# Kernel optimization log

Hardware: AMD Instinct MI355X
Metric: run time of the kernel (lower is better)

Reference implementation:

```python
import jax, jax.numpy as jnp
import numpy as np

# --- batched state-vector quantum circuit sim: AngleEmbedding(RY) + BasicEntanglerLayers(RX + ring CNOT) ---

def _ry(state, theta, wire, n):
    # per-sample RY(theta) on `wire`; state: (B,) + (2,)*n complex
    ax = wire + 1
    c = jnp.cos(0.5 * theta).reshape((-1,) + (1,) * (n - 1)).astype(state.dtype)
    s = jnp.sin(0.5 * theta).reshape((-1,) + (1,) * (n - 1)).astype(state.dtype)
    s0 = jnp.take(state, 0, axis=ax)
    s1 = jnp.take(state, 1, axis=ax)
    return jnp.stack([c * s0 - s * s1, s * s0 + c * s1], axis=ax)

def _rx(state, theta, wire, n):
    # scalar RX(theta) on `wire` (shared weight across batch)
    ax = wire + 1
    c = jnp.cos(0.5 * theta).astype(state.dtype)
    s = (-1j * jnp.sin(0.5 * theta)).astype(state.dtype)
    s0 = jnp.take(state, 0, axis=ax)
    s1 = jnp.take(state, 1, axis=ax)
    return jnp.stack([c * s0 + s * s1, s * s0 + c * s1], axis=ax)

def _cnot(state, ctrl, tgt):
    ax_c = ctrl + 1
    s0 = jnp.take(state, 0, axis=ax_c)
    s1 = jnp.take(state, 1, axis=ax_c)
    ax_t = tgt + 1 if tgt < ctrl else tgt  # target axis index after removing ctrl axis
    s1 = jnp.flip(s1, axis=ax_t)
    return jnp.stack([s0, s1], axis=ax_c)

def _circuit(x_qin, qweights):
    # x_qin: (Bn, n) angles; qweights: (L, n)
    Bn, n = x_qin.shape
    state = jnp.zeros((Bn,) + (2,) * n, jnp.complex64)
    state = state.at[(slice(None),) + (0,) * n].set(1.0)
    for w in range(n):  # AngleEmbedding, rotation='Y'
        state = _ry(state, x_qin[:, w], w, n)
    for l in range(qweights.shape[0]):  # BasicEntanglerLayers
        for w in range(n):
            state = _rx(state, qweights[l, w], w, n)
        for w in range(n):
            state = _cnot(state, w, (w + 1) % n)
    probs = jnp.real(state * jnp.conj(state))
    outs = []
    for w in range(n):  # <Z_w> = P(bit_w=0) - P(bit_w=1)
        axes = tuple(a for a in range(1, n + 1) if a != w + 1)
        p = probs.sum(axis=axes)  # (Bn, 2)
        outs.append(p[:, 0] - p[:, 1])
    return jnp.stack(outs, axis=-1).astype(jnp.float32)


def setup_inputs() -> dict:
    key = jax.random.key(0)
    ks = jax.random.split(key, 9)
    B, N, H, NQ, L = 16, 1024, 256, 8, 2
    x = jax.random.normal(ks[0], (B, N, H), jnp.float32)
    norm_adj = jax.random.uniform(ks[1], (N, N), jnp.float32) / N
    Wg = jax.random.normal(ks[2], (H, H), jnp.float32) * 0.02
    bg = jax.random.normal(ks[3], (H,), jnp.float32) * 0.02
    Wpre = jax.random.normal(ks[4], (NQ, H), jnp.float32) * 0.05
    bpre = jax.random.normal(ks[5], (NQ,), jnp.float32) * 0.02
    qweights = jax.random.uniform(ks[6], (L, NQ), jnp.float32) * (2.0 * np.pi)
    Wpost = jax.random.normal(ks[7], (H, NQ), jnp.float32) * 0.1
    bpost = jax.random.normal(ks[8], (H,), jnp.float32) * 0.02
    return {"x": x, "norm_adj": norm_adj, "Wg": Wg, "bg": bg, "Wpre": Wpre,
            "bpre": bpre, "qweights": qweights, "Wpost": Wpost, "bpost": bpost}


def reference(x, norm_adj, Wg, bg, Wpre, bpre, qweights, Wpost, bpost):
    # GCN aggregation + GELU(Linear)  (dropout is identity in eval mode)
    x_agg = jnp.einsum('ij,bjh->bih', norm_adj, x)
    x_agg = jax.nn.gelu(x_agg @ Wg.T + bg, approximate=False)
    B, N, H = x_agg.shape
    x_flat = x_agg.reshape(B * N, H).astype(jnp.float32)
    x_qin = jnp.tanh(x_flat @ Wpre.T + bpre) * np.pi
    q_out = _circuit(x_qin, qweights)          # (B*N, n_qubits)
    out = (q_out @ Wpost.T + bpost).reshape(B, N, H)
    return out
```

## Files before the change

kernel.cpp:

```cpp
#include <hip/hip_runtime.h>
#include <math.h>

typedef __attribute__((ext_vector_type(8))) short bf16x8;
typedef _Float16 f16x8 __attribute__((ext_vector_type(8)));
typedef __attribute__((ext_vector_type(4))) float f32x4;

#define PI_F 3.14159265358979323846f

__device__ __forceinline__ unsigned short f2bf(float f) {
  unsigned int u = __float_as_uint(f);
  u += 0x7FFFu + ((u >> 16) & 1u);
  return (unsigned short)(u >> 16);
}

__device__ __forceinline__ float bf2f(unsigned short u) {
  return __uint_as_float(((unsigned int)u) << 16);
}

__device__ __forceinline__ void async_ld16(const unsigned short* g, unsigned short* l) {
  __builtin_amdgcn_global_load_lds(
      (const __attribute__((address_space(1))) void*)g,
      (__attribute__((address_space(3))) void*)l,
      16, 0, 0);
}

__device__ __forceinline__ float fast_erf(float x) {
  float a = fabsf(x);
  float t = 1.0f / fmaf(0.3275911f, a, 1.0f);
  float p = t * fmaf(t, fmaf(t, fmaf(t, fmaf(t, 1.061405429f, -1.453152027f),
                                     1.421413741f), -0.284496736f), 0.254829592f);
  float e = __expf(-a * a);
  float r = 1.0f - p * e;
  return copysignf(r, x);
}

__device__ __forceinline__ float fast_tanh(float a) {
  float e = __expf(2.0f * a);
  return 1.0f - 2.0f / (e + 1.0f);
}

template<int ML, int MR>
__device__ __forceinline__ void apply_rx(float re[4], float im[4], float c, float s) {
  float pr[4], pi[4];
  #pragma unroll
  for (int r = 0; r < 4; r++) {
    float vr = re[r ^ MR], vi = im[r ^ MR];
    if (ML) { vr = __shfl_xor(vr, ML, 64); vi = __shfl_xor(vi, ML, 64); }
    pr[r] = vr; pi[r] = vi;
  }
  #pragma unroll
  for (int r = 0; r < 4; r++) {
    re[r] = fmaf(c, re[r],  s * pi[r]);
    im[r] = fmaf(c, im[r], -s * pr[r]);
  }
}

__device__ __forceinline__ void fold_reduce8(float v[8], int L) {
  #pragma unroll
  for (int step = 0; step < 3; step++) {
    int d = 1 << step;
    int half = 4 >> step;
    bool hi = (L & d) != 0;
    #pragma unroll
    for (int w = 0; w < half; w++) {
      float send = hi ? v[w] : v[w + half];
      float recv = __shfl_xor(send, d, 64);
      v[w] = (hi ? v[w + half] : v[w]) + recv;
    }
  }
  v[0] += __shfl_xor(v[0], 8, 64);
  v[0] += __shfl_xor(v[0], 16, 64);
  v[0] += __shfl_xor(v[0], 32, 64);
}

__global__ __launch_bounds__(256)
void prep_kernel(const float* __restrict__ adj, unsigned short* __restrict__ adj_bf,
                 const float* __restrict__ Wg, unsigned short* __restrict__ Wg_bf,
                 const float* __restrict__ qw, unsigned short* __restrict__ Uri,
                 const float* __restrict__ Wpost, _Float16* __restrict__ Gt,
                 const float* __restrict__ x, unsigned short* __restrict__ xT) {
  __shared__ float smem[1056];
  int bid = blockIdx.x, t = threadIdx.x;
  if (bid < 1024) {
    int i = bid * 256 + t;
    float4 v = ((const float4*)adj)[i];
    ushort4 o; o.x = f2bf(v.x); o.y = f2bf(v.y); o.z = f2bf(v.z); o.w = f2bf(v.w);
    ((ushort4*)adj_bf)[i] = o;
  } else if (bid < 1088) {
    int i = (bid - 1024) * 256 + t;
    float4 v = ((const float4*)Wg)[i];
    ushort4 o; o.x = f2bf(v.x); o.y = f2bf(v.y); o.z = f2bf(v.z); o.w = f2bf(v.w);
    ((ushort4*)Wg_bf)[i] = o;
  } else if (bid < 1152) {
    if (t < 16) { smem[t] = cosf(0.5f * qw[t]); smem[16 + t] = sinf(0.5f * qw[t]); }
    __syncthreads();
    int wv = t >> 6, L = t & 63;
    int k = (bid - 1088) * 4 + wv;
    float re[4], im[4];
    #pragma unroll
    for (int r = 0; r < 4; r++) { re[r] = (r * 64 + L == k) ? 1.f : 0.f; im[r] = 0.f; }
    apply_rx<1, 0>(re, im, smem[0], smem[16]);
    apply_rx<2, 0>(re, im, smem[1], smem[17]);
    apply_rx<4, 0>(re, im, smem[2], smem[18]);
    apply_rx<8, 0>(re, im, smem[3], smem[19]);
    apply_rx<16, 0>(re, im, smem[4], smem[20]);
    apply_rx<32, 0>(re, im, smem[5], smem[21]);
    apply_rx<0, 1>(re, im, smem[6], smem[22]);
    apply_rx<0, 2>(re, im, smem[7], smem[23]);
    apply_rx<3, 0>(re, im, smem[8], smem[24]);
    apply_rx<6, 0>(re, im, smem[9], smem[25]);
    apply_rx<12, 0>(re, im, smem[10], smem[26]);
    apply_rx<24, 0>(re, im, smem[11], smem[27]);
    apply_rx<48, 0>(re, im, smem[12], smem[28]);
    apply_rx<32, 1>(re, im, smem[13], smem[29]);
    apply_rx<0, 3>(re, im, smem[14], smem[30]);
    apply_rx<3, 2>(re, im, smem[15], smem[31]);
    const int M[8] = {0xAB, 0xFD, 0xFA, 0xF5, 0xEA, 0xD5, 0xAA, 0x55};
    #pragma unroll
    for (int r = 0; r < 4; r++) {
      int n = 0;
      #pragma unroll
      for (int w = 0; w < 8; w++) {
        int bit = (__popc(L & (M[w] & 63)) ^ __popc((r << 6) & M[w])) & 1;
        n |= bit << w;
      }
      int row_re = ((n >> 4) << 5) + (n & 15);
      Uri[(size_t)row_re * 256 + k] = f2bf(re[r]);
      Uri[(size_t)(row_re + 16) * 256 + k] = f2bf(im[r]);
    }
  } else if (bid < 1168) {
    int tid = (bid - 1152) * 256 + t;
    int h = tid >> 4;
    int n0 = (tid & 15) << 4;
    float wv8[8];
    #pragma unroll
    for (int w = 0; w < 8; w++) wv8[w] = Wpost[h * 8 + w];
    #pragma unroll
    for (int j = 0; j < 16; j++) {
      int n = n0 + j;
      float sum = 0.f;
      #pragma unroll
      for (int w = 0; w < 8; w++) sum += ((n >> w) & 1) ? -wv8[w] : wv8[w];
      Gt[h * 256 + n] = (_Float16)sum;
    }
  } else {
    int tb = bid - 1168;
    int jt = tb & 31, ht = (tb >> 5) & 7, bb = tb >> 8;
    int tx = t & 31, ty = t >> 5;
    const float* xb = x + (size_t)bb * 1024 * 256;
    #pragma unroll
    for (int i = 0; i < 4; i++) {
      int j = jt * 32 + ty + i * 8;
      smem[(ty + i * 8) * 33 + tx] = xb[(size_t)j * 256 + ht * 32 + tx];
    }
    __syncthreads();
    unsigned short* xTb = xT + (size_t)bb * 256 * 1024;
    #pragma unroll
    for (int i = 0; i < 4; i++) {
      int h = ht * 32 + ty + i * 8;
      xTb[(size_t)h * 1024 + jt * 32 + tx] = f2bf(smem[tx * 33 + ty + i * 8]);
    }
  }
}

__global__ __launch_bounds__(256)
void gemm1_kernel(const unsigned short* __restrict__ A,
                  const unsigned short* __restrict__ Bt,
                  unsigned short* __restrict__ C,
                  int K, int tilesN, int ldC) {
  __shared__ unsigned short As[2 * 128 * 32];
  __shared__ unsigned short Bs[2 * 64 * 32];
  int rr  = blockIdx.x;
  int im  = rr / tilesN;
  int in_ = rr % tilesN;
  const unsigned short* Ab  = A  + (long long)im * 128 * K;
  const unsigned short* Btb = Bt + (long long)in_ * 64 * K;

  int t = threadIdx.x;
  int wv = t >> 6, lane = t & 63;
  int wm = wv >> 1, wn = wv & 1;
  int l15 = lane & 15, quad = lane >> 4;

  f32x4 acc[4][2] = {};

  for (int kk = 0; kk < K; kk += 64) {
    __syncthreads();
    #pragma unroll
    for (int kb = 0; kb < 2; kb++) {
      #pragma unroll
      for (int q = 0; q < 2; q++) {
        int ch = q * 256 + t;
        async_ld16(Ab + (long long)(ch >> 2) * K + kk + kb * 32 + (ch & 3) * 8,
                   &As[kb * 4096 + ch * 8]);
      }
      {
        int ch = t;
        async_ld16(Btb + (long long)(ch >> 2) * K + kk + kb * 32 + (ch & 3) * 8,
                   &Bs[kb * 2048 + ch * 8]);
      }
    }
    __syncthreads();
    #pragma unroll
    for (int kb = 0; kb < 2; kb++) {
      bf16x8 af[4], bfr[2];
      #pragma unroll
      for (int mt = 0; mt < 4; mt++)
        af[mt] = *(const bf16x8*)&As[kb * 4096 + (wm * 64 + mt * 16 + l15) * 32 + quad * 8];
      #pragma unroll
      for (int nt = 0; nt < 2; nt++)
        bfr[nt] = *(const bf16x8*)&Bs[kb * 2048 + (wn * 32 + nt * 16 + l15) * 32 + quad * 8];
      #pragma unroll
      for (int mt = 0; mt < 4; mt++)
        #pragma unroll
        for (int nt = 0; nt < 2; nt++)
          acc[mt][nt] = __builtin_amdgcn_mfma_f32_16x16x32_bf16(af[mt], bfr[nt], acc[mt][nt], 0, 0, 0);
    }
  }

  int n0 = in_ * 64;
  #pragma unroll
  for (int mt = 0; mt < 4; mt++) {
    #pragma unroll
    for (int nt = 0; nt < 2; nt++) {
      int colg = n0 + wn * 32 + nt * 16 + l15;
      #pragma unroll
      for (int r = 0; r < 4; r++) {
        int rowg = im * 128 + wm * 64 + mt * 16 + quad * 4 + r;
        C[(size_t)rowg * ldC + colg] = f2bf(acc[mt][nt][r]);
      }
    }
  }
}

__global__ __launch_bounds__(256)
void qfused_kernel(const unsigned short* __restrict__ xagg,
                   const unsigned short* __restrict__ Wg,
                   const float* __restrict__ bg,
                   const float* __restrict__ Wpre, const float* __restrict__ bpre,
                   const unsigned short* __restrict__ Uri,
                   const _Float16* __restrict__ Gt,
                   const float* __restrict__ bpost,
                   float* __restrict__ out) {
  __shared__ __align__(16) char smemraw[75776];
  unsigned short* As    = (unsigned short*)smemraw;
  unsigned short* Bs    = (unsigned short*)(smemraw + 2048);
  unsigned short* gs    = (unsigned short*)(smemraw + 34816);
  _Float16*       Ts    = (_Float16*)(smemraw + 34816);
  unsigned short* P0s   = (unsigned short*)(smemraw + 51200);
  float*          sWpre = (float*)(smemraw + 67584);

  int t = threadIdx.x;
  int wv = t >> 6, lane = t & 63;
  int l15 = lane & 15, quad = lane >> 4;

  for (int i = t; i < 2048; i += 256) sWpre[i] = Wpre[i];

  const unsigned short* Ab = xagg + (size_t)blockIdx.x * 32 * 256;

  f32x4 acc[2][4] = {};
  for (int kk = 0; kk < 256; kk += 32) {
    __syncthreads();
    if (wv < 2)
      async_ld16(Ab + (size_t)(wv * 16 + (lane >> 2)) * 256 + kk + (lane & 3) * 8,
                 &As[(wv * 16) * 32]);
    #pragma unroll
    for (int rd = 0; rd < 4; rd++) {
      int n = wv * 64 + rd * 16 + (lane >> 2);
      async_ld16(Wg + (size_t)n * 256 + kk + (lane & 3) * 8,
                 &Bs[(wv * 64 + rd * 16) * 32]);
    }
    __syncthreads();
    bf16x8 af[2], bfr[4];
    #pragma unroll
    for (int mt = 0; mt < 2; mt++)
      af[mt] = *(const bf16x8*)&As[(mt * 16 + l15) * 32 + quad * 8];
    #pragma unroll
    for (int nt = 0; nt < 4; nt++)
      bfr[nt] = *(const bf16x8*)&Bs[(wv * 64 + nt * 16 + l15) * 32 + quad * 8];
    #pragma unroll
    for (int mt = 0; mt < 2; mt++)
      #pragma unroll
      for (int nt = 0; nt < 4; nt++)
        acc[mt][nt] = __builtin_amdgcn_mfma_f32_16x16x32_bf16(af[mt], bfr[nt], acc[mt][nt], 0, 0, 0);
  }
  #pragma unroll
  for (int mt = 0; mt < 2; mt++) {
    #pragma unroll
    for (int nt = 0; nt < 4; nt++) {
      int col = wv * 64 + nt * 16 + l15;
      float bgl = bg[col];
      #pragma unroll
      for (int r = 0; r < 4; r++) {
        int row = mt * 16 + quad * 4 + r;
        float v = acc[mt][nt][r] + bgl;
        v = 0.5f * v * (1.0f + fast_erf(v * 0.7071067811865475f));
        gs[row * 256 + col] = f2bf(v);
      }
    }
  }
  __syncthreads();

  #pragma unroll
  for (int rr = 0; rr < 8; rr++) {
    int row = wv * 8 + rr;
    ushort4 gu = *(const ushort4*)&gs[row * 256 + 4 * lane];
    float g0 = bf2f(gu.x), g1 = bf2f(gu.y), g2 = bf2f(gu.z), g3 = bf2f(gu.w);
    float ang[8];
    #pragma unroll
    for (int w = 0; w < 8; w++) {
      float4 wp = *(const float4*)&sWpre[w * 256 + 4 * lane];
      float a = g0 * wp.x;
      a = fmaf(g1, wp.y, a);
      a = fmaf(g2, wp.z, a);
      a = fmaf(g3, wp.w, a);
      ang[w] = a;
    }
    fold_reduce8(ang, lane);
    float angf[8];
    #pragma unroll
    for (int w = 0; w < 8; w++) {
      int src = ((w >> 2) & 1) | (w & 2) | ((w & 1) << 2);
      angf[w] = __shfl(ang[0], src, 64);
    }
    float cw[8], sw[8];
    #pragma unroll
    for (int w = 0; w < 8; w++) {
      float th = (0.5f * PI_F) * fast_tanh(angf[w] + bpre[w]);
      cw[w] = __cosf(th); sw[w] = __sinf(th);
    }
    float pl = 1.f;
    #pragma unroll
    for (int bbit = 0; bbit < 6; bbit++) pl *= ((lane >> bbit) & 1) ? sw[bbit + 2] : cw[bbit + 2];
    ushort4 o;
    o.x = f2bf(pl * cw[0] * cw[1]);
    o.y = f2bf(pl * sw[0] * cw[1]);
    o.z = f2bf(pl * cw[0] * sw[1]);
    o.w = f2bf(pl * sw[0] * sw[1]);
    *(ushort4*)&P0s[(lane >> 3) * 1024 + row * 32 + 4 * (lane & 7)] = o;
  }

  f32x4 acc1[2][8] = {};
  for (int kk = 0; kk < 256; kk += 32) {
    __syncthreads();
    #pragma unroll
    for (int rd = 0; rd < 8; rd++) {
      int n = wv * 128 + rd * 16 + (lane >> 2);
      async_ld16(Uri + (size_t)n * 256 + kk + (lane & 3) * 8,
                 &Bs[(wv * 128 + rd * 16) * 32]);
    }
    __syncthreads();
    bf16x8 af[2], bfr[8];
    #pragma unroll
    for (int mt = 0; mt < 2; mt++)
      af[mt] = *(const bf16x8*)&P0s[(kk >> 5) * 1024 + (mt * 16 + l15) * 32 + quad * 8];
    #pragma unroll
    for (int nt = 0; nt < 8; nt++)
      bfr[nt] = *(const bf16x8*)&Bs[(wv * 128 + nt * 16 + l15) * 32 + quad * 8];
    #pragma unroll
    for (int mt = 0; mt < 2; mt++)
      #pragma unroll
      for (int nt = 0; nt < 8; nt++)
        acc1[mt][nt] = __builtin_amdgcn_mfma_f32_16x16x32_bf16(af[mt], bfr[nt], acc1[mt][nt], 0, 0, 0);
  }

  #pragma unroll
  for (int mt = 0; mt < 2; mt++) {
    #pragma unroll
    for (int p = 0; p < 4; p++) {
      int kb = wv * 2 + (p >> 1);
      int cip = (p & 1) * 16 + l15;
      #pragma unroll
      for (int r = 0; r < 4; r++) {
        int row = mt * 16 + quad * 4 + r;
        float tre = acc1[mt][2 * p][r], tim = acc1[mt][2 * p + 1][r];
        Ts[kb * 1024 + row * 32 + cip] = (_Float16)(tre * tre + tim * tim);
      }
    }
  }

  f32x4 acc2[2][4] = {};
  for (int kk = 0; kk < 256; kk += 32) {
    __syncthreads();
    #pragma unroll
    for (int rd = 0; rd < 4; rd++) {
      int h = wv * 64 + rd * 16 + (lane >> 2);
      async_ld16((const unsigned short*)Gt + (size_t)h * 256 + kk + (lane & 3) * 8,
                 &Bs[(wv * 64 + rd * 16) * 32]);
    }
    __syncthreads();
    f16x8 af[2], bfr[4];
    #pragma unroll
    for (int mt = 0; mt < 2; mt++)
      af[mt] = *(const f16x8*)&Ts[(kk >> 5) * 1024 + (mt * 16 + l15) * 32 + quad * 8];
    #pragma unroll
    for (int nt = 0; nt < 4; nt++)
      bfr[nt] = *(const f16x8*)&Bs[(wv * 64 + nt * 16 + l15) * 32 + quad * 8];
    #pragma unroll
    for (int mt = 0; mt < 2; mt++)
      #pragma unroll
      for (int nt = 0; nt < 4; nt++)
        acc2[mt][nt] = __builtin_amdgcn_mfma_f32_16x16x32_f16(af[mt], bfr[nt], acc2[mt][nt], 0, 0, 0);
  }

  #pragma unroll
  for (int mt = 0; mt < 2; mt++) {
    #pragma unroll
    for (int nt = 0; nt < 4; nt++) {
      int col = wv * 64 + nt * 16 + l15;
      float bp = bpost[col];
      #pragma unroll
      for (int r = 0; r < 4; r++) {
        int row = mt * 16 + quad * 4 + r;
        int s = blockIdx.x * 32 + row;
        int orow = (s & 15) * 1024 + (s >> 4);
        out[(size_t)orow * 256 + col] = acc2[mt][nt][r] + bp;
      }
    }
  }
}

extern "C" void kernel_launch(void* const* d_in, const int* in_sizes, int n_in,
                              void* d_out, int out_size, void* d_ws, size_t ws_size,
                              hipStream_t stream) {
  const float* x     = (const float*)d_in[0];
  const float* adj   = (const float*)d_in[1];
  const float* Wg    = (const float*)d_in[2];
  const float* bg    = (const float*)d_in[3];
  const float* Wpre  = (const float*)d_in[4];
  const float* bpre  = (const float*)d_in[5];
  const float* qw    = (const float*)d_in[6];
  const float* Wpost = (const float*)d_in[7];
  const float* bpost = (const float*)d_in[8];
  float* out = (float*)d_out;

  char* ws = (char*)d_ws;
  unsigned short* adj_bf  = (unsigned short*)(ws + 0);
  unsigned short* Wg_bf   = (unsigned short*)(ws + 2097152);
  unsigned short* xT_bf   = (unsigned short*)(ws + 2228224);
  unsigned short* xagg_bf = (unsigned short*)(ws + 10616832);
  unsigned short* Uri     = (unsigned short*)(ws + 19005440);
  _Float16*       Gt      = (_Float16*)(ws + 19267584);

  prep_kernel<<<5264, 256, 0, stream>>>(adj, adj_bf, Wg, Wg_bf, qw, Uri,
                                        Wpost, Gt, x, xT_bf);

  gemm1_kernel<<<512, 256, 0, stream>>>(adj_bf, xT_bf, xagg_bf, 1024, 64, 4096);

  qfused_kernel<<<512, 256, 0, stream>>>(xagg_bf, Wg_bf, bg, Wpre, bpre, Uri, Gt, bpost, out);
}
```

Measured before the change: 146.9 us.

## Load GEMM operands directly from global into registers with double buffering, swizzle LDS

In the fused quantum kernel, the three GEMM stages now load their B-operand weights (and the A operand of the first stage) straight from global memory into registers, double-buffered one k-step ahead. This replaces the async global-to-LDS copies and the two barriers per k-step. Wpre is held in registers rather than LDS, and tanh/cos/sin is computed once per lane and then shuffled instead of being repeated eight times per lane. The P0 and T intermediate LDS tiles use an XOR swizzle to reduce bank conflicts, and LDS use drops from about 74KB to 32KB, which may allow more blocks per CU at the cost of higher register pressure and uncoalesced weight loads that depend on L2 hits.

```diff
diff --git a/kernel.cpp b/kernel.cpp
--- a/kernel.cpp
+++ b/kernel.cpp
@@ -241,47 +241,43 @@
                    const _Float16* __restrict__ Gt,
                    const float* __restrict__ bpost,
                    float* __restrict__ out) {
-  __shared__ __align__(16) char smemraw[75776];
-  unsigned short* As    = (unsigned short*)smemraw;
-  unsigned short* Bs    = (unsigned short*)(smemraw + 2048);
-  unsigned short* gs    = (unsigned short*)(smemraw + 34816);
-  _Float16*       Ts    = (_Float16*)(smemraw + 34816);
-  unsigned short* P0s   = (unsigned short*)(smemraw + 51200);
-  float*          sWpre = (float*)(smemraw + 67584);
+  __shared__ __align__(16) char smemraw[32768];
+  unsigned short* gs  = (unsigned short*)smemraw;
+  _Float16*       Ts  = (_Float16*)smemraw;
+  unsigned short* P0s = (unsigned short*)(smemraw + 16384);
 
   int t = threadIdx.x;
   int wv = t >> 6, lane = t & 63;
   int l15 = lane & 15, quad = lane >> 4;
 
-  for (int i = t; i < 2048; i += 256) sWpre[i] = Wpre[i];
-
   const unsigned short* Ab = xagg + (size_t)blockIdx.x * 32 * 256;
 
   f32x4 acc[2][4] = {};
-  for (int kk = 0; kk < 256; kk += 32) {
-    __syncthreads();
-    if (wv < 2)
-      async_ld16(Ab + (size_t)(wv * 16 + (lane >> 2)) * 256 + kk + (lane & 3) * 8,
-                 &As[(wv * 16) * 32]);
-    #pragma unroll
-    for (int rd = 0; rd < 4; rd++) {
-      int n = wv * 64 + rd * 16 + (lane >> 2);
-      async_ld16(Wg + (size_t)n * 256 + kk + (lane & 3) * 8,
-                 &Bs[(wv * 64 + rd * 16) * 32]);
-    }
-    __syncthreads();
-    bf16x8 af[2], bfr[4];
-    #pragma unroll
-    for (int mt = 0; mt < 2; mt++)
-      af[mt] = *(const bf16x8*)&As[(mt * 16 + l15) * 32 + quad * 8];
-    #pragma unroll
-    for (int nt = 0; nt < 4; nt++)
-      bfr[nt] = *(const bf16x8*)&Bs[(wv * 64 + nt * 16 + l15) * 32 + quad * 8];
-    #pragma unroll
-    for (int mt = 0; mt < 2; mt++)
-      #pragma unroll
-      for (int nt = 0; nt < 4; nt++)
-        acc[mt][nt] = __builtin_amdgcn_mfma_f32_16x16x32_bf16(af[mt], bfr[nt], acc[mt][nt], 0, 0, 0);
+  {
+    const unsigned short* Ap = Ab + (size_t)l15 * 256 + quad * 8;
+    const unsigned short* Wp = Wg + (size_t)(wv * 64 + l15) * 256 + quad * 8;
+    bf16x8 af[2][2], wf[2][4];
+    #pragma unroll
+    for (int mt = 0; mt < 2; mt++) af[0][mt] = *(const bf16x8*)(Ap + mt * 4096);
+    #pragma unroll
+    for (int nt = 0; nt < 4; nt++) wf[0][nt] = *(const bf16x8*)(Wp + nt * 4096);
+    #pragma unroll
+    for (int k8 = 0; k8 < 8; k8++) {
+      int cur = k8 & 1, nxt = cur ^ 1;
+      if (k8 < 7) {
+        #pragma unroll
+        for (int mt = 0; mt < 2; mt++)
+          af[nxt][mt] = *(const bf16x8*)(Ap + (k8 + 1) * 32 + mt * 4096);
+        #pragma unroll
+        for (int nt = 0; nt < 4; nt++)
+          wf[nxt][nt] = *(const bf16x8*)(Wp + (k8 + 1) * 32 + nt * 4096);
+      }
+      #pragma unroll
+      for (int mt = 0; mt < 2; mt++)
+        #pragma unroll
+        for (int nt = 0; nt < 4; nt++)
+          acc[mt][nt] = __builtin_amdgcn_mfma_f32_16x16x32_bf16(af[cur][mt], wf[cur][nt], acc[mt][nt], 0, 0, 0);
+    }
   }
   #pragma unroll
   for (int mt = 0; mt < 2; mt++) {
@@ -298,6 +294,10 @@
       }
     }
   }
+  float4 wp[8];
+  #pragma unroll
+  for (int w = 0; w < 8; w++) wp[w] = *(const float4*)&Wpre[w * 256 + 4 * lane];
+  float bprel = bpre[4 * (lane & 1) + (lane & 2) + ((lane >> 2) & 1)];
   __syncthreads();
 
   #pragma unroll
@@ -308,59 +308,63 @@
     float ang[8];
     #pragma unroll
     for (int w = 0; w < 8; w++) {
-      float4 wp = *(const float4*)&sWpre[w * 256 + 4 * lane];
-      float a = g0 * wp.x;
-      a = fmaf(g1, wp.y, a);
-      a = fmaf(g2, wp.z, a);
-      a = fmaf(g3, wp.w, a);
+      float4 w4 = wp[w];
+      float a = g0 * w4.x;
+      a = fmaf(g1, w4.y, a);
+      a = fmaf(g2, w4.z, a);
+      a = fmaf(g3, w4.w, a);
       ang[w] = a;
     }
     fold_reduce8(ang, lane);
-    float angf[8];
+    float th = (0.5f * PI_F) * fast_tanh(ang[0] + bprel);
+    float c = __cosf(th), s = __sinf(th);
+    float cw[8], sw[8];
     #pragma unroll
     for (int w = 0; w < 8; w++) {
       int src = ((w >> 2) & 1) | (w & 2) | ((w & 1) << 2);
-      angf[w] = __shfl(ang[0], src, 64);
-    }
-    float cw[8], sw[8];
-    #pragma unroll
-    for (int w = 0; w < 8; w++) {
-      float th = (0.5f * PI_F) * fast_tanh(angf[w] + bpre[w]);
-      cw[w] = __cosf(th); sw[w] = __sinf(th);
+      cw[w] = __shfl(c, src, 64);
+      sw[w] = __shfl(s, src, 64);
     }
     float pl = 1.f;
     #pragma unroll
-    for (int bbit = 0; bbit < 6; bbit++) pl *= ((lane >> bbit) & 1) ? sw[bbit + 2] : cw[bbit + 2];
+    for (int b = 0; b < 6; b++) pl *= ((lane >> b) & 1) ? sw[b + 2] : cw[b + 2];
     ushort4 o;
     o.x = f2bf(pl * cw[0] * cw[1]);
     o.y = f2bf(pl * sw[0] * cw[1]);
     o.z = f2bf(pl * cw[0] * sw[1]);
     o.w = f2bf(pl * sw[0] * sw[1]);
-    *(ushort4*)&P0s[(lane >> 3) * 1024 + row * 32 + 4 * (lane & 7)] = o;
-  }
+    int j = lane & 7;
+    int cswz = (j >> 1) ^ ((row >> 1) & 3);
+    *(ushort4*)((char*)P0s + (lane >> 3) * 2048 + row * 64 + cswz * 16 + (j & 1) * 8) = o;
+  }
+  __syncthreads();
 
   f32x4 acc1[2][8] = {};
-  for (int kk = 0; kk < 256; kk += 32) {
-    __syncthreads();
-    #pragma unroll
-    for (int rd = 0; rd < 8; rd++) {
-      int n = wv * 128 + rd * 16 + (lane >> 2);
-      async_ld16(Uri + (size_t)n * 256 + kk + (lane & 3) * 8,
-                 &Bs[(wv * 128 + rd * 16) * 32]);
-    }
-    __syncthreads();
-    bf16x8 af[2], bfr[8];
-    #pragma unroll
-    for (int mt = 0; mt < 2; mt++)
-      af[mt] = *(const bf16x8*)&P0s[(kk >> 5) * 1024 + (mt * 16 + l15) * 32 + quad * 8];
-    #pragma unroll
-    for (int nt = 0; nt < 8; nt++)
-      bfr[nt] = *(const bf16x8*)&Bs[(wv * 128 + nt * 16 + l15) * 32 + quad * 8];
-    #pragma unroll
-    for (int mt = 0; mt < 2; mt++)
-      #pragma unroll
-      for (int nt = 0; nt < 8; nt++)
-        acc1[mt][nt] = __builtin_amdgcn_mfma_f32_16x16x32_bf16(af[mt], bfr[nt], acc1[mt][nt], 0, 0, 0);
+  {
+    const unsigned short* Up = Uri + (size_t)(wv * 128 + l15) * 256 + quad * 8;
+    const char* Pp = (const char*)P0s + l15 * 64 + (((quad ^ ((l15 >> 1) & 3))) << 4);
+    bf16x8 pa[2][2], ua[2][8];
+    #pragma unroll
+    for (int mt = 0; mt < 2; mt++) pa[0][mt] = *(const bf16x8*)(Pp + mt * 1024);
+    #pragma unroll
+    for (int nt = 0; nt < 8; nt++) ua[0][nt] = *(const bf16x8*)(Up + nt * 4096);
+    #pragma unroll
+    for (int k8 = 0; k8 < 8; k8++) {
+      int cur = k8 & 1, nxt = cur ^ 1;
+      if (k8 < 7) {
+        #pragma unroll
+        for (int mt = 0; mt < 2; mt++)
+          pa[nxt][mt] = *(const bf16x8*)(Pp + (k8 + 1) * 2048 + mt * 1024);
+        #pragma unroll
+        for (int nt = 0; nt < 8; nt++)
+          ua[nxt][nt] = *(const bf16x8*)(Up + (k8 + 1) * 32 + nt * 4096);
+      }
+      #pragma unroll
+      for (int mt = 0; mt < 2; mt++)
+        #pragma unroll
+        for (int nt = 0; nt < 8; nt++)
+          acc1[mt][nt] = __builtin_amdgcn_mfma_f32_16x16x32_bf16(pa[cur][mt], ua[cur][nt], acc1[mt][nt], 0, 0, 0);
+    }
   }
 
   #pragma unroll
@@ -369,37 +373,45 @@
     for (int p = 0; p < 4; p++) {
       int kb = wv * 2 + (p >> 1);
       int cip = (p & 1) * 16 + l15;
+      int ch = cip >> 3;
       #pragma unroll
       for (int r = 0; r < 4; r++) {
         int row = mt * 16 + quad * 4 + r;
         float tre = acc1[mt][2 * p][r], tim = acc1[mt][2 * p + 1][r];
-        Ts[kb * 1024 + row * 32 + cip] = (_Float16)(tre * tre + tim * tim);
-      }
-    }
-  }
+        *(_Float16*)((char*)Ts + kb * 2048 + row * 64 +
+                     ((ch ^ ((row >> 1) & 3)) << 4) + (cip & 7) * 2)
+            = (_Float16)(tre * tre + tim * tim);
+      }
+    }
+  }
+  __syncthreads();
 
   f32x4 acc2[2][4] = {};
-  for (int kk = 0; kk < 256; kk += 32) {
-    __syncthreads();
-    #pragma unroll
-    for (int rd = 0; rd < 4; rd++) {
-      int h = wv * 64 + rd * 16 + (lane >> 2);
-      async_ld16((const unsigned short*)Gt + (size_t)h * 256 + kk + (lane & 3) * 8,
-                 &Bs[(wv * 64 + rd * 16) * 32]);
-    }
-    __syncthreads();
-    f16x8 af[2], bfr[4];
-    #pragma unroll
-    for (int mt = 0; mt < 2; mt++)
-      af[mt] = *(const f16x8*)&Ts[(kk >> 5) * 1024 + (mt * 16 + l15) * 32 + quad * 8];
-    #pragma unroll
-    for (int nt = 0; nt < 4; nt++)
-      bfr[nt] = *(const f16x8*)&Bs[(wv * 64 + nt * 16 + l15) * 32 + quad * 8];
-    #pragma unroll
-    for (int mt = 0; mt < 2; mt++)
-      #pragma unroll
-      for (int nt = 0; nt < 4; nt++)
-        acc2[mt][nt] = __builtin_amdgcn_mfma_f32_16x16x32_f16(af[mt], bfr[nt], acc2[mt][nt], 0, 0, 0);
+  {
+    const _Float16* Gp = Gt + (size_t)(wv * 64 + l15) * 256 + quad * 8;
+    const char* Tp = (const char*)Ts + l15 * 64 + (((quad ^ ((l15 >> 1) & 3))) << 4);
+    f16x8 tf[2][2], gf[2][4];
+    #pragma unroll
+    for (int mt = 0; mt < 2; mt++) tf[0][mt] = *(const f16x8*)(Tp + mt * 1024);
+    #pragma unroll
+    for (int nt = 0; nt < 4; nt++) gf[0][nt] = *(const f16x8*)(Gp + nt * 4096);
+    #pragma unroll
+    for (int k8 = 0; k8 < 8; k8++) {
+      int cur = k8 & 1, nxt = cur ^ 1;
+      if (k8 < 7) {
+        #pragma unroll
+        for (int mt = 0; mt < 2; mt++)
+          tf[nxt][mt] = *(const f16x8*)(Tp + (k8 + 1) * 2048 + mt * 1024);
+        #pragma unroll
+        for (int nt = 0; nt < 4; nt++)
+          gf[nxt][nt] = *(const f16x8*)(Gp + (k8 + 1) * 32 + nt * 4096);
+      }
+      #pragma unroll
+      for (int mt = 0; mt < 2; mt++)
+        #pragma unroll
+        for (int nt = 0; nt < 4; nt++)
+          acc2[mt][nt] = __builtin_amdgcn_mfma_f32_16x16x32_f16(tf[cur][mt], gf[cur][nt], acc2[mt][nt], 0, 0, 0);
+    }
   }
 
   #pragma unroll
```

Measured after the change: 149.1 us. About the same (+1.4%).
